# Performance work log

Measured on AMD Instinct MI355X. Metric: run time of the kernel, lower is better.

Reference implementation:

```python
import jax, jax.numpy as jnp
import numpy as np

B, H, W, C = 4, 64, 64, 1024
REF_FRAC = 0.05


def setup_inputs() -> dict:
    key = jax.random.key(0)
    k1, k2 = jax.random.split(key)
    embeddings = jax.random.normal(k1, (B, H, W, C), dtype=jnp.float32)
    # sparse boolean reference masks, guaranteed non-empty per item
    ref_masks = jax.random.uniform(k2, (B, H, W)) < REF_FRAC
    ref_masks = ref_masks.at[:, 0, 0].set(True)
    return {"embeddings": embeddings, "ref_masks": ref_masks}


def reference(embeddings, ref_masks):
    """Fixed-shape JAX translation of InstanceMatcher.forward_match.

    Instead of per-item argwhere/dynamic gather, we compute the full NxN
    cosine-similarity matrix and express the ref/remaining partition with
    boolean masks. Returns:
      match  : [B, N, N] bool  -- match[b, i, j] True iff patch i is a ref patch,
               patch j is a non-ref patch, and sim > per-item median threshold
               (equivalent to the rows of the original `maps_to` output; global
               flat indices i, j map to coords via (i // W, i % W)).
      sim    : [B, N, N] float -- cosine similarities (all pairs).
      thresh : [B] float       -- median-of-max threshold per item.
    """
    Bn, Hn, Wn, Cn = embeddings.shape
    N = Hn * Wn
    x = embeddings.reshape(Bn, N, Cn)
    m = ref_masks.reshape(Bn, N)  # [B, N] bool, True = ref patch

    # F.normalize(x, dim=-1): x / max(||x||, eps)
    norm = jnp.linalg.norm(x, axis=-1, keepdims=True)
    fn = x / jnp.maximum(norm, 1e-12)

    # all-pairs cosine similarity; only (ref row, non-ref col) entries are used
    sim = jnp.einsum('bnc,bmc->bnm', fn, fn)  # [B, N, N]

    valid = m[:, :, None] & (~m)[:, None, :]  # [B, N, N]

    # max over remaining (non-ref) columns, per ref row
    max_per_ref = jnp.max(jnp.where(valid, sim, -jnp.inf), axis=2)  # [B, N]

    # torch.median (lower median) over the ref rows only: sort with non-ref
    # rows pushed to +inf, then pick element (k-1)//2 where k = #ref patches
    vals = jnp.where(m, max_per_ref, jnp.inf)
    vals_sorted = jnp.sort(vals, axis=1)
    k = jnp.sum(m, axis=1)  # [B]
    med_idx = (k - 1) // 2
    thresh = jnp.take_along_axis(vals_sorted, med_idx[:, None], axis=1)[:, 0]  # [B]

    match = valid & (sim > thresh[:, None, None])
    return match, sim, thresh
```

## Files before the change

kernel.cpp:

```cpp
#include <hip/hip_runtime.h>
#include <hip/hip_bf16.h>
#include <stdint.h>
#include <math.h>

#define BQ 4
#define NQ 4096
#define CQ 1024

#define WS_CTR      0
#define WS_THRESH   64
#define WS_MASK     256
#define WS_REFIDX   17408
#define WS_MAXV     82944
#define WS_FNH      (4u << 20)
#define WS_FNL      (WS_FNH + (32u << 20))
#define WS_NEED     (WS_FNL + (32u << 20) + (1u << 20))

typedef __bf16 bf16x8 __attribute__((ext_vector_type(8)));
typedef float floatx4 __attribute__((ext_vector_type(4)));

__global__ void k_detect(const uint8_t* mraw, int* ctr) {
    int c123 = 0, c3f = 0;
    for (int i = threadIdx.x; i < BQ * NQ; i += blockDim.x) {
        uint8_t v = mraw[i];
        int m4 = i & 3;
        if (m4 != 0 && v != 0) c123++;
        if (m4 == 3 && v == 0x3F) c3f++;
    }
    atomicAdd(&ctr[0], c123);
    atomicAdd(&ctr[1], c3f);
}

__global__ void k_canon(const void* mraw, const int* ctr, uint8_t* maskc) {
    int i = blockIdx.x * blockDim.x + threadIdx.x;
    if (i >= BQ * NQ) return;
    int c123 = ctr[0], c3f = ctr[1];
    uint8_t v;
    if (c3f > 64) {
        v = (((const float*)mraw)[i] != 0.0f) ? 1 : 0;
    } else if (c123 == 0) {
        v = (((const int*)mraw)[i] != 0) ? 1 : 0;
    } else {
        v = (((const uint8_t*)mraw)[i] != 0) ? 1 : 0;
    }
    maskc[i] = v;
}

__global__ void k_compact(const uint8_t* maskc, int* refCount, int* refIdx) {
    int b = blockIdx.x;
    for (int i = threadIdx.x; i < NQ; i += blockDim.x) {
        if (maskc[b * NQ + i]) {
            int p = atomicAdd(&refCount[b], 1);
            refIdx[b * NQ + p] = i;
        }
    }
}

__global__ __launch_bounds__(128) void k_prep(const float* x, __bf16* fnh, __bf16* fnl) {
    int row = blockIdx.x;
    int t = threadIdx.x;
    const float4* xr = (const float4*)(x + (long long)row * CQ);
    float4 a = xr[t * 2 + 0];
    float4 c = xr[t * 2 + 1];
    double s = (double)a.x * a.x + (double)a.y * a.y + (double)a.z * a.z + (double)a.w * a.w
             + (double)c.x * c.x + (double)c.y * c.y + (double)c.z * c.z + (double)c.w * c.w;
    __shared__ double red[128];
    __shared__ double invs;
    red[t] = s;
    __syncthreads();
    for (int o = 64; o > 0; o >>= 1) {
        if (t < o) red[t] += red[t + o];
        __syncthreads();
    }
    if (t == 0) invs = 1.0 / fmax(sqrt(red[0]), 1e-12);
    __syncthreads();
    float ir = (float)invs;
    float v[8] = {a.x, a.y, a.z, a.w, c.x, c.y, c.z, c.w};
    bf16x8 h8, l8;
#pragma unroll
    for (int j = 0; j < 8; j++) {
        float xn = v[j] * ir;
        __bf16 h = (__bf16)xn;
        h8[j] = h;
        l8[j] = (__bf16)(xn - (float)h);
    }
    *(bf16x8*)(fnh + (long long)row * CQ + t * 8) = h8;
    *(bf16x8*)(fnl + (long long)row * CQ + t * 8) = l8;
}

#define GRID_MEGA 2112
__global__ __launch_bounds__(256) void k_mega(const __bf16* fnh, const __bf16* fnl,
                                              float* sim, float* match) {
    __shared__ __align__(16) char smem[32768];
    const int id = blockIdx.x;
    const int gid = (id & 7) * 264 + (id >> 3);
    const int b = gid / 528;
    int rem = gid % 528;
    int rT = 0;
    while (rem >= 32 - rT) { rem -= 32 - rT; rT++; }
    const int cT = rT + rem;
    const int rowBase = rT * 128;
    const int colBase = cT * 128;
    const __bf16* baseh = fnh + (long long)b * NQ * CQ;
    const __bf16* basel = fnl + (long long)b * NQ * CQ;
    __bf16* smAh = (__bf16*)smem;
    __bf16* smAl = (__bf16*)(smem + 8192);
    __bf16* smBh = (__bf16*)(smem + 16384);
    __bf16* smBl = (__bf16*)(smem + 24576);

    const int lane = threadIdx.x & 63;
    const int w = threadIdx.x >> 6;
    const int wr = w >> 1, wc = w & 1;
    const int ldrow = lane >> 2;
    const int ldcolS = ((lane & 3) * 8) ^ (((lane >> 3) & 3) << 3);
    const int co = ((lane >> 4) * 8) ^ (((lane >> 1) & 3) << 3);

    floatx4 acc[4][4] = {};

    for (int k0 = 0; k0 < CQ; k0 += 32) {
        __syncthreads();
#pragma unroll
        for (int i = 0; i < 2; i++) {
            int rsub = w * 16 + i * 64;
            long long offA = (long long)(rowBase + rsub + ldrow) * CQ + k0 + ldcolS;
            long long offB = (long long)(colBase + rsub + ldrow) * CQ + k0 + ldcolS;
            __builtin_amdgcn_global_load_lds(
                (const __attribute__((address_space(1))) void*)(baseh + offA),
                (__attribute__((address_space(3))) void*)(smAh + rsub * 32), 16, 0, 0);
            __builtin_amdgcn_global_load_lds(
                (const __attribute__((address_space(1))) void*)(basel + offA),
                (__attribute__((address_space(3))) void*)(smAl + rsub * 32), 16, 0, 0);
            __builtin_amdgcn_global_load_lds(
                (const __attribute__((address_space(1))) void*)(baseh + offB),
                (__attribute__((address_space(3))) void*)(smBh + rsub * 32), 16, 0, 0);
            __builtin_amdgcn_global_load_lds(
                (const __attribute__((address_space(1))) void*)(basel + offB),
                (__attribute__((address_space(3))) void*)(smBl + rsub * 32), 16, 0, 0);
        }
        __syncthreads();

        bf16x8 ah[4], al[4];
#pragma unroll
        for (int i = 0; i < 4; i++) {
            int ra = (wr * 64 + i * 16 + (lane & 15)) * 32 + co;
            ah[i] = *(const bf16x8*)(smAh + ra);
            al[i] = *(const bf16x8*)(smAl + ra);
        }
#pragma unroll
        for (int j = 0; j < 4; j++) {
            int rb = (wc * 64 + j * 16 + (lane & 15)) * 32 + co;
            bf16x8 bh = *(const bf16x8*)(smBh + rb);
            bf16x8 bl = *(const bf16x8*)(smBl + rb);
#pragma unroll
            for (int i = 0; i < 4; i++) {
                acc[i][j] = __builtin_amdgcn_mfma_f32_16x16x32_bf16(ah[i], bh, acc[i][j], 0, 0, 0);
                acc[i][j] = __builtin_amdgcn_mfma_f32_16x16x32_bf16(ah[i], bl, acc[i][j], 0, 0, 0);
                acc[i][j] = __builtin_amdgcn_mfma_f32_16x16x32_bf16(al[i], bh, acc[i][j], 0, 0, 0);
            }
        }
    }

    float* simb = sim + (long long)b * NQ * NQ;
    float* matb = match + (long long)b * NQ * NQ;
#pragma unroll
    for (int i = 0; i < 4; i++) {
        int r0 = rowBase + wr * 64 + i * 16 + (lane >> 4) * 4;
#pragma unroll
        for (int r = 0; r < 4; r++) {
#pragma unroll
            for (int j = 0; j < 4; j++) {
                int c = colBase + wc * 64 + j * 16 + (lane & 15);
                simb[(long long)(r0 + r) * NQ + c] = acc[i][j][r];
                matb[(long long)(r0 + r) * NQ + c] = 0.0f;
            }
        }
    }
    if (rT != cT) {
        floatx4 zero4 = {0.0f, 0.0f, 0.0f, 0.0f};
#pragma unroll
        for (int i = 0; i < 4; i++) {
            int r0 = rowBase + wr * 64 + i * 16 + (lane >> 4) * 4;
#pragma unroll
            for (int j = 0; j < 4; j++) {
                int c = colBase + wc * 64 + j * 16 + (lane & 15);
                long long off = (long long)c * NQ + r0;
                *(floatx4*)(simb + off) = acc[i][j];
                *(floatx4*)(matb + off) = zero4;
            }
        }
    }
}

__global__ __launch_bounds__(256) void k_rowmax(const float* sim, const uint8_t* maskc,
                                                const int* refCount, const int* refIdx,
                                                float* maxv) {
    int b = blockIdx.y;
    int cnt = refCount[b];
    __shared__ float red[256];
    for (int slot = blockIdx.x; slot < cnt; slot += gridDim.x) {
        int row = refIdx[b * NQ + slot];
        const float* rp = sim + ((long long)b * NQ + row) * NQ;
        float mx = -INFINITY;
        for (int j = threadIdx.x; j < NQ; j += 256) {
            if (!maskc[b * NQ + j]) mx = fmaxf(mx, rp[j]);
        }
        __syncthreads();
        red[threadIdx.x] = mx;
        __syncthreads();
        for (int o = 128; o > 0; o >>= 1) {
            if (threadIdx.x < o) red[threadIdx.x] = fmaxf(red[threadIdx.x], red[threadIdx.x + o]);
            __syncthreads();
        }
        if (threadIdx.x == 0) maxv[b * NQ + slot] = red[0];
    }
}

__global__ __launch_bounds__(256) void k_median(const float* maxv, const int* refCount,
                                                float* threshv, float* outth) {
    int b = blockIdx.x;
    int k = refCount[b];
    __shared__ float vals[NQ];
    __shared__ float result;
    for (int i = threadIdx.x; i < k; i += blockDim.x) vals[i] = maxv[b * NQ + i];
    __syncthreads();
    int med = (k - 1) / 2;
    for (int t0 = threadIdx.x; t0 < k; t0 += blockDim.x) {
        float v = vals[t0];
        int cl = 0, ce = 0;
        for (int j = 0; j < k; j++) {
            float w = vals[j];
            cl += (w < v) ? 1 : 0;
            ce += (w == v) ? 1 : 0;
        }
        if (cl <= med && med < cl + ce) result = v;
    }
    __syncthreads();
    if (threadIdx.x == 0) {
        threshv[b] = result;
        outth[b] = result;
    }
}

__global__ __launch_bounds__(256) void k_match(const float* sim, const uint8_t* maskc,
                                               const int* refCount, const int* refIdx,
                                               const float* threshv, float* match) {
    int b = blockIdx.y;
    int cnt = refCount[b];
    float th = threshv[b];
    const uint8_t* mb = maskc + b * NQ;
    for (int slot = blockIdx.x; slot < cnt; slot += gridDim.x) {
        int row = refIdx[b * NQ + slot];
        const float* rp = sim + ((long long)b * NQ + row) * NQ;
        float* op = match + ((long long)b * NQ + row) * NQ;
        for (int j = threadIdx.x * 4; j < NQ; j += 256 * 4) {
            float4 s = *(const float4*)(rp + j);
            float4 o;
            o.x = (!mb[j + 0] && s.x > th) ? 1.0f : 0.0f;
            o.y = (!mb[j + 1] && s.y > th) ? 1.0f : 0.0f;
            o.z = (!mb[j + 2] && s.z > th) ? 1.0f : 0.0f;
            o.w = (!mb[j + 3] && s.w > th) ? 1.0f : 0.0f;
            *(float4*)(op + j) = o;
        }
    }
}

extern "C" void kernel_launch(void* const* d_in, const int* in_sizes, int n_in,
                              void* d_out, int out_size, void* d_ws, size_t ws_size,
                              hipStream_t stream) {
    if (in_sizes[0] != BQ * NQ * CQ) return;
    if (ws_size < WS_NEED) return;

    const float* x = (const float*)d_in[0];
    const void* mraw = d_in[1];
    float* out = (float*)d_out;
    uint8_t* ws = (uint8_t*)d_ws;

    int* ctr       = (int*)(ws + WS_CTR);
    int* refCount  = (int*)(ws + 16);
    float* threshv = (float*)(ws + WS_THRESH);
    uint8_t* maskc = ws + WS_MASK;
    int* refIdx    = (int*)(ws + WS_REFIDX);
    float* maxv    = (float*)(ws + WS_MAXV);
    __bf16* fnh    = (__bf16*)(ws + WS_FNH);
    __bf16* fnl    = (__bf16*)(ws + WS_FNL);

    float* match = out;
    float* sim   = out + (long long)BQ * NQ * NQ;
    float* outth = out + 2LL * BQ * NQ * NQ;

    hipMemsetAsync(ws, 0, 4096, stream);

    k_detect<<<1, 256, 0, stream>>>((const uint8_t*)mraw, ctr);
    k_canon<<<(BQ * NQ + 255) / 256, 256, 0, stream>>>(mraw, ctr, maskc);
    k_compact<<<BQ, 256, 0, stream>>>(maskc, refCount, refIdx);
    k_prep<<<BQ * NQ, 128, 0, stream>>>(x, fnh, fnl);
    k_mega<<<GRID_MEGA, 256, 0, stream>>>(fnh, fnl, sim, match);
    k_rowmax<<<dim3(256, BQ), 256, 0, stream>>>(sim, maskc, refCount, refIdx, maxv);
    k_median<<<BQ, 256, 0, stream>>>(maxv, refCount, threshv, outth);
    k_match<<<dim3(256, BQ), 256, 0, stream>>>(sim, maskc, refCount, refIdx, threshv, match);
}
```

Measured before the change: 825.5 us.

## Double-buffer LDS tiles in k_mega to overlap global loads with MFMA

Changes the GEMM main loop from single-buffered LDS staging with two syncthreads per k-step to a double-buffered scheme. The next k-slice is prefetched with global_load_lds while MFMAs run on the current buffer, using explicit vmcnt waits and raw s_barrier. The aim is to hide global memory latency behind compute. LDS use doubles to 64KB per block, which may reduce occupancy. The hand-placed waitcnt and barrier ordering also risks subtle races.

```diff
diff --git a/kernel.cpp b/kernel.cpp
--- a/kernel.cpp
+++ b/kernel.cpp
@@ -89,9 +89,14 @@
 }
 
 #define GRID_MEGA 2112
+
+#define GLD(src, dst) __builtin_amdgcn_global_load_lds( \
+    (const __attribute__((address_space(1))) void*)(src), \
+    (__attribute__((address_space(3))) void*)(dst), 16, 0, 0)
+
 __global__ __launch_bounds__(256) void k_mega(const __bf16* fnh, const __bf16* fnl,
                                               float* sim, float* match) {
-    __shared__ __align__(16) char smem[32768];
+    __shared__ __align__(16) __bf16 sm[32768];
     const int id = blockIdx.x;
     const int gid = (id & 7) * 264 + (id >> 3);
     const int b = gid / 528;
@@ -103,10 +108,6 @@
     const int colBase = cT * 128;
     const __bf16* baseh = fnh + (long long)b * NQ * CQ;
     const __bf16* basel = fnl + (long long)b * NQ * CQ;
-    __bf16* smAh = (__bf16*)smem;
-    __bf16* smAl = (__bf16*)(smem + 8192);
-    __bf16* smBh = (__bf16*)(smem + 16384);
-    __bf16* smBl = (__bf16*)(smem + 24576);
 
     const int lane = threadIdx.x & 63;
     const int w = threadIdx.x >> 6;
@@ -115,42 +116,48 @@
     const int ldcolS = ((lane & 3) * 8) ^ (((lane >> 3) & 3) << 3);
     const int co = ((lane >> 4) * 8) ^ (((lane >> 1) & 3) << 3);
 
+    const int rs0 = w * 16, rs1 = w * 16 + 64;
+    const long long gA0 = (long long)(rowBase + rs0 + ldrow) * CQ + ldcolS;
+    const long long gA1 = (long long)(rowBase + rs1 + ldrow) * CQ + ldcolS;
+    const long long gB0 = (long long)(colBase + rs0 + ldrow) * CQ + ldcolS;
+    const long long gB1 = (long long)(colBase + rs1 + ldrow) * CQ + ldcolS;
+
     floatx4 acc[4][4] = {};
 
-    for (int k0 = 0; k0 < CQ; k0 += 32) {
-        __syncthreads();
-#pragma unroll
-        for (int i = 0; i < 2; i++) {
-            int rsub = w * 16 + i * 64;
-            long long offA = (long long)(rowBase + rsub + ldrow) * CQ + k0 + ldcolS;
-            long long offB = (long long)(colBase + rsub + ldrow) * CQ + k0 + ldcolS;
-            __builtin_amdgcn_global_load_lds(
-                (const __attribute__((address_space(1))) void*)(baseh + offA),
-                (__attribute__((address_space(3))) void*)(smAh + rsub * 32), 16, 0, 0);
-            __builtin_amdgcn_global_load_lds(
-                (const __attribute__((address_space(1))) void*)(basel + offA),
-                (__attribute__((address_space(3))) void*)(smAl + rsub * 32), 16, 0, 0);
-            __builtin_amdgcn_global_load_lds(
-                (const __attribute__((address_space(1))) void*)(baseh + offB),
-                (__attribute__((address_space(3))) void*)(smBh + rsub * 32), 16, 0, 0);
-            __builtin_amdgcn_global_load_lds(
-                (const __attribute__((address_space(1))) void*)(basel + offB),
-                (__attribute__((address_space(3))) void*)(smBl + rsub * 32), 16, 0, 0);
-        }
-        __syncthreads();
+#define STAGE(k0, buf) do {                                   \
+        GLD(baseh + gA0 + (k0), (buf) + 0     + rs0 * 32);    \
+        GLD(baseh + gA1 + (k0), (buf) + 0     + rs1 * 32);    \
+        GLD(basel + gA0 + (k0), (buf) + 4096  + rs0 * 32);    \
+        GLD(basel + gA1 + (k0), (buf) + 4096  + rs1 * 32);    \
+        GLD(baseh + gB0 + (k0), (buf) + 8192  + rs0 * 32);    \
+        GLD(baseh + gB1 + (k0), (buf) + 8192  + rs1 * 32);    \
+        GLD(basel + gB0 + (k0), (buf) + 12288 + rs0 * 32);    \
+        GLD(basel + gB1 + (k0), (buf) + 12288 + rs1 * 32);    \
+    } while (0)
+
+    STAGE(0, sm);
+    for (int t = 0; t < 32; t++) {
+        __bf16* cur = sm + (t & 1) * 16384;
+        if (t < 31) {
+            STAGE((t + 1) * 32, sm + ((t + 1) & 1) * 16384);
+            asm volatile("s_waitcnt vmcnt(8)" ::: "memory");
+        } else {
+            asm volatile("s_waitcnt vmcnt(0)" ::: "memory");
+        }
+        __builtin_amdgcn_s_barrier();
 
         bf16x8 ah[4], al[4];
 #pragma unroll
         for (int i = 0; i < 4; i++) {
             int ra = (wr * 64 + i * 16 + (lane & 15)) * 32 + co;
-            ah[i] = *(const bf16x8*)(smAh + ra);
-            al[i] = *(const bf16x8*)(smAl + ra);
+            ah[i] = *(const bf16x8*)(cur + ra);
+            al[i] = *(const bf16x8*)(cur + 4096 + ra);
         }
 #pragma unroll
         for (int j = 0; j < 4; j++) {
             int rb = (wc * 64 + j * 16 + (lane & 15)) * 32 + co;
-            bf16x8 bh = *(const bf16x8*)(smBh + rb);
-            bf16x8 bl = *(const bf16x8*)(smBl + rb);
+            bf16x8 bh = *(const bf16x8*)(cur + 8192 + rb);
+            bf16x8 bl = *(const bf16x8*)(cur + 12288 + rb);
 #pragma unroll
             for (int i = 0; i < 4; i++) {
                 acc[i][j] = __builtin_amdgcn_mfma_f32_16x16x32_bf16(ah[i], bh, acc[i][j], 0, 0, 0);
@@ -158,7 +165,10 @@
                 acc[i][j] = __builtin_amdgcn_mfma_f32_16x16x32_bf16(al[i], bh, acc[i][j], 0, 0, 0);
             }
         }
-    }
+        asm volatile("s_waitcnt lgkmcnt(0)" ::: "memory");
+        __builtin_amdgcn_s_barrier();
+    }
+#undef STAGE
 
     float* simb = sim + (long long)b * NQ * NQ;
     float* matb = match + (long long)b * NQ * NQ;
```

Measured after the change: 837.5 us. About the same (+1.4%).
